# Optimization experiments

Measured on AMD Instinct MI355X. Metric: run time of the kernel, lower is better.

Reference implementation:

```python
import jax, jax.numpy as jnp
import numpy as np

ALPHAS = (0.1, 0.3, 0.5)
WEIGHTS = (0.5, 0.3, 0.2)

B, T, D = 32, 8192, 64


def setup_inputs() -> dict:
    key = jax.random.key(0)
    k1, k2 = jax.random.split(key)
    pred = jax.random.normal(k1, (B, T, D), dtype=jnp.float32)
    target = jax.random.normal(k2, (B, T, D), dtype=jnp.float32)
    return {"pred": pred, "target": target}


def _ema(x, alpha):
    # ema_0 = x_0 ; ema_i = alpha*x_i + (1-alpha)*ema_{i-1}
    # Express each step as affine op (mult, add) and compose with an
    # associative scan along the time axis (dim=1):  y_i = mult*y_{i-1} + add.
    mult = jnp.full(x.shape, 1.0 - alpha, dtype=x.dtype).at[:, 0].set(0.0)
    add = (alpha * x).at[:, 0].set(x[:, 0])

    def combine(c1, c2):  # apply c1 first, then c2
        a1, b1 = c1
        a2, b2 = c2
        return (a1 * a2, b1 * a2 + b2)

    _, ema = jax.lax.associative_scan(combine, (mult, add), axis=1)
    return ema


def _scale_loss(pred, target, alpha):
    pe = _ema(pred, alpha)   # [B, T, D]
    te = _ema(target, alpha)
    pd = pe[:, 1:] - pe[:, :-1]
    td = te[:, 1:] - te[:, :-1]
    mismatch = jnp.sign(pd) != jnp.sign(td)
    step_err = jnp.square(pe[:, 1:] - te[:, 1:])
    masked = jnp.where(mismatch, step_err, jnp.zeros_like(step_err))
    return masked.mean(axis=1)  # [B, D]


def reference(pred, target):
    loss = sum(w * _scale_loss(pred, target, a) for a, w in zip(ALPHAS, WEIGHTS))
    return loss.mean()  # reduction='mean'
```

## Files before the change

kernel.cpp:

```cpp
#include <hip/hip_runtime.h>


namespace {
constexpr int BB  = 32;
constexpr int TT  = 8192;
constexpr int DD  = 64;
constexpr int CH  = 64;
constexpr int WU  = 32;
constexpr int NCH = TT / CH;
constexpr int WPB = 4;
constexpr int BT  = 16;
constexpr float INV_NORM = 1.0f / (8191.0f * 2048.0f);
}

__global__ void zero_out_kernel(float* o) { o[0] = 0.0f; }

__device__ __forceinline__ void load16(const float* __restrict__ p,
                                       const float* __restrict__ q, int bt,
                                       float (&xs)[BT], float (&ys)[BT]) {
#pragma unroll
  for (int i = 0; i < BT; ++i) {
    xs[i] = p[(bt + i) * DD];
    ys[i] = q[(bt + i) * DD];
  }
}

__device__ __forceinline__ void warm16_a0(const float (&xs)[BT], const float (&ys)[BT],
                                          float& pe0, float& te0) {
#pragma unroll
  for (int i = 0; i < BT; ++i) {
    pe0 = fmaf(0.1f, xs[i] - pe0, pe0);
    te0 = fmaf(0.1f, ys[i] - te0, te0);
  }
}

__device__ __forceinline__ void warm16_all(const float (&xs)[BT], const float (&ys)[BT],
    float& pe0, float& te0, float& pe1, float& te1, float& pe2, float& te2) {
#pragma unroll
  for (int i = 0; i < BT; ++i) {
    pe0 = fmaf(0.1f, xs[i] - pe0, pe0);  te0 = fmaf(0.1f, ys[i] - te0, te0);
    pe1 = fmaf(0.3f, xs[i] - pe1, pe1);  te1 = fmaf(0.3f, ys[i] - te1, te1);
    pe2 = fmaf(0.5f, xs[i] - pe2, pe2);  te2 = fmaf(0.5f, ys[i] - te2, te2);
  }
}

__device__ __forceinline__ void step1(float xx, float yy, float a, float w,
                                      float& pe, float& te, float& acc) {
  float dx = xx - pe;
  float dy = yy - te;
  pe = fmaf(a, dx, pe);
  te = fmaf(a, dy, te);
  float e   = pe - te;
  float sel = (dx * dy < 0.0f) ? w : 0.0f;
  acc = fmaf(sel, e * e, acc);
}

__device__ __forceinline__ void acc16_all(const float (&xs)[BT], const float (&ys)[BT],
    float& pe0, float& te0, float& pe1, float& te1, float& pe2, float& te2,
    float& acc) {
#pragma unroll
  for (int i = 0; i < BT; ++i) {
    step1(xs[i], ys[i], 0.1f, 0.5f, pe0, te0, acc);
    step1(xs[i], ys[i], 0.3f, 0.3f, pe1, te1, acc);
    step1(xs[i], ys[i], 0.5f, 0.2f, pe2, te2, acc);
  }
}

__global__ __launch_bounds__(256, 4) void ms_trend_loss_kernel(
    const float* __restrict__ pred, const float* __restrict__ targ,
    float* __restrict__ out) {
  const int lane = threadIdx.x & 63;
  const int wave = threadIdx.x >> 6;
  const int unit = blockIdx.x * WPB + wave;
  const int b = unit >> 7;
  const int c = unit & 127;
  const int s = c * CH;
  const int start = (c == 0) ? 0 : (s - WU);

  const float* p = pred + (b * TT + start) * DD + lane;
  const float* q = targ + (b * TT + start) * DD + lane;

  float pe0, pe1, pe2, te0, te1, te2;
  float acc = 0.0f;
  float xa[BT], ya[BT], xb[BT], yb[BT];

  if (c == 0) {
    load16(p, q, 0, xa, ya);
    load16(p, q, BT, xb, yb);
    pe0 = pe1 = pe2 = xa[0];
    te0 = te1 = te2 = ya[0];
    acc16_all(xa, ya, pe0, te0, pe1, te1, pe2, te2, acc);
    load16(p, q, 2 * BT, xa, ya);
    acc16_all(xb, yb, pe0, te0, pe1, te1, pe2, te2, acc);
    load16(p, q, 3 * BT, xb, yb);
    acc16_all(xa, ya, pe0, te0, pe1, te1, pe2, te2, acc);
    acc16_all(xb, yb, pe0, te0, pe1, te1, pe2, te2, acc);
  } else {
    load16(p, q, 0, xa, ya);
    load16(p, q, BT, xb, yb);
    pe0 = xa[0];
    te0 = ya[0];
    warm16_a0(xa, ya, pe0, te0);
    load16(p, q, 2 * BT, xa, ya);
    pe1 = pe2 = xb[0];
    te1 = te2 = yb[0];
    warm16_all(xb, yb, pe0, te0, pe1, te1, pe2, te2);
    load16(p, q, 3 * BT, xb, yb);
    acc16_all(xa, ya, pe0, te0, pe1, te1, pe2, te2, acc);
    load16(p, q, 4 * BT, xa, ya);
    acc16_all(xb, yb, pe0, te0, pe1, te1, pe2, te2, acc);
    load16(p, q, 5 * BT, xb, yb);
    acc16_all(xa, ya, pe0, te0, pe1, te1, pe2, te2, acc);
    acc16_all(xb, yb, pe0, te0, pe1, te1, pe2, te2, acc);
  }

#pragma unroll
  for (int off = 32; off > 0; off >>= 1) acc += __shfl_down(acc, off);
  __shared__ float sred[WPB];
  if (lane == 0) sred[wave] = acc;
  __syncthreads();
  if (threadIdx.x == 0) {
    float t = sred[0] + sred[1] + sred[2] + sred[3];
    atomicAdd(out, t * INV_NORM);
  }
}

extern "C" void kernel_launch(void* const* d_in, const int* in_sizes, int n_in,
                              void* d_out, int out_size, void* d_ws, size_t ws_size,
                              hipStream_t stream) {
  (void)in_sizes; (void)n_in; (void)out_size; (void)d_ws; (void)ws_size;
  const float* pred = (const float*)d_in[0];
  const float* targ = (const float*)d_in[1];
  float* out = (float*)d_out;

  zero_out_kernel<<<1, 1, 0, stream>>>(out);
  ms_trend_loss_kernel<<<BB * NCH / WPB, 256, 0, stream>>>(pred, targ, out);
}
```

Before: 146.3 us.

## Stream inputs through LDS via async global_load_lds double buffering

Replaces per-lane register loads of 16-row batches with asynchronous global-to-LDS copies (16-byte per lane) into a per-wave double-buffered shared tile of 8 rows. Each wave waits on vmcnt, runs the EMA recurrence reading from LDS, then issues the next batch. The goal is wider, fully coalesced loads with fewer VGPRs and better overlap of memory and compute. The cost is extra LDS traffic, explicit waitcnt handling, and the occupancy hint being dropped from launch bounds.

```diff
diff --git a/kernel.cpp b/kernel.cpp
--- a/kernel.cpp
+++ b/kernel.cpp
@@ -9,38 +9,51 @@
 constexpr int WU  = 32;
 constexpr int NCH = TT / CH;
 constexpr int WPB = 4;
-constexpr int BT  = 16;
+constexpr int BT  = 8;
 constexpr float INV_NORM = 1.0f / (8191.0f * 2048.0f);
 }
 
+typedef const __attribute__((address_space(1))) void* gas_ptr;
+typedef __attribute__((address_space(3))) void* las_ptr;
+
 __global__ void zero_out_kernel(float* o) { o[0] = 0.0f; }
 
-__device__ __forceinline__ void load16(const float* __restrict__ p,
-                                       const float* __restrict__ q, int bt,
-                                       float (&xs)[BT], float (&ys)[BT]) {
+#define WAIT_V4() do { asm volatile("s_waitcnt vmcnt(4)" ::: "memory"); \
+                       __builtin_amdgcn_sched_barrier(0); } while (0)
+#define WAIT_V0() do { asm volatile("s_waitcnt vmcnt(0)" ::: "memory"); \
+                       __builtin_amdgcn_sched_barrier(0); } while (0)
+#define WAIT_LG() do { asm volatile("s_waitcnt lgkmcnt(0)" ::: "memory"); \
+                       __builtin_amdgcn_sched_barrier(0); } while (0)
+
+__device__ __forceinline__ void issue_batch(const float* gx, const float* gy,
+                                            float* lx, float* ly) {
 #pragma unroll
-  for (int i = 0; i < BT; ++i) {
-    xs[i] = p[(bt + i) * DD];
-    ys[i] = q[(bt + i) * DD];
+  for (int r = 0; r < 2; ++r) {
+    __builtin_amdgcn_global_load_lds((gas_ptr)(gx + r * 4 * DD),
+                                     (las_ptr)(lx + r * 4 * DD), 16, 0, 0);
+    __builtin_amdgcn_global_load_lds((gas_ptr)(gy + r * 4 * DD),
+                                     (las_ptr)(ly + r * 4 * DD), 16, 0, 0);
   }
 }
 
-__device__ __forceinline__ void warm16_a0(const float (&xs)[BT], const float (&ys)[BT],
-                                          float& pe0, float& te0) {
+__device__ __forceinline__ void warm8_a0(const float* tx, const float* ty,
+                                         float& pe0, float& te0) {
 #pragma unroll
   for (int i = 0; i < BT; ++i) {
-    pe0 = fmaf(0.1f, xs[i] - pe0, pe0);
-    te0 = fmaf(0.1f, ys[i] - te0, te0);
+    float xx = tx[i * DD], yy = ty[i * DD];
+    pe0 = fmaf(0.1f, xx - pe0, pe0);
+    te0 = fmaf(0.1f, yy - te0, te0);
   }
 }
 
-__device__ __forceinline__ void warm16_all(const float (&xs)[BT], const float (&ys)[BT],
+__device__ __forceinline__ void warm8_all(const float* tx, const float* ty,
     float& pe0, float& te0, float& pe1, float& te1, float& pe2, float& te2) {
 #pragma unroll
   for (int i = 0; i < BT; ++i) {
-    pe0 = fmaf(0.1f, xs[i] - pe0, pe0);  te0 = fmaf(0.1f, ys[i] - te0, te0);
-    pe1 = fmaf(0.3f, xs[i] - pe1, pe1);  te1 = fmaf(0.3f, ys[i] - te1, te1);
-    pe2 = fmaf(0.5f, xs[i] - pe2, pe2);  te2 = fmaf(0.5f, ys[i] - te2, te2);
+    float xx = tx[i * DD], yy = ty[i * DD];
+    pe0 = fmaf(0.1f, xx - pe0, pe0);  te0 = fmaf(0.1f, yy - te0, te0);
+    pe1 = fmaf(0.3f, xx - pe1, pe1);  te1 = fmaf(0.3f, yy - te1, te1);
+    pe2 = fmaf(0.5f, xx - pe2, pe2);  te2 = fmaf(0.5f, yy - te2, te2);
   }
 }
 
@@ -55,20 +68,22 @@
   acc = fmaf(sel, e * e, acc);
 }
 
-__device__ __forceinline__ void acc16_all(const float (&xs)[BT], const float (&ys)[BT],
+__device__ __forceinline__ void acc8(const float* tx, const float* ty,
     float& pe0, float& te0, float& pe1, float& te1, float& pe2, float& te2,
     float& acc) {
 #pragma unroll
   for (int i = 0; i < BT; ++i) {
-    step1(xs[i], ys[i], 0.1f, 0.5f, pe0, te0, acc);
-    step1(xs[i], ys[i], 0.3f, 0.3f, pe1, te1, acc);
-    step1(xs[i], ys[i], 0.5f, 0.2f, pe2, te2, acc);
+    float xx = tx[i * DD], yy = ty[i * DD];
+    step1(xx, yy, 0.1f, 0.5f, pe0, te0, acc);
+    step1(xx, yy, 0.3f, 0.3f, pe1, te1, acc);
+    step1(xx, yy, 0.5f, 0.2f, pe2, te2, acc);
   }
 }
 
-__global__ __launch_bounds__(256, 4) void ms_trend_loss_kernel(
-    const float* __restrict__ pred, const float* __restrict__ targ,
-    float* __restrict__ out) {
+__global__ void __launch_bounds__(256)
+ms_trend_loss_kernel(const float* __restrict__ pred,
+                     const float* __restrict__ targ,
+                     float* __restrict__ out) {
   const int lane = threadIdx.x & 63;
   const int wave = threadIdx.x >> 6;
   const int unit = blockIdx.x * WPB + wave;
@@ -77,41 +92,69 @@
   const int s = c * CH;
   const int start = (c == 0) ? 0 : (s - WU);
 
-  const float* p = pred + (b * TT + start) * DD + lane;
-  const float* q = targ + (b * TT + start) * DD + lane;
+  const float* gx = pred + (b * TT + start) * DD + lane * 4;
+  const float* gy = targ + (b * TT + start) * DD + lane * 4;
+
+  __shared__ float tile[WPB][2][2][BT * DD];
+#define LX(k) (&tile[wave][(k) & 1][0][0])
+#define LY(k) (&tile[wave][(k) & 1][1][0])
+#define TX(k) (&tile[wave][(k) & 1][0][lane])
+#define TY(k) (&tile[wave][(k) & 1][1][lane])
 
   float pe0, pe1, pe2, te0, te1, te2;
   float acc = 0.0f;
-  float xa[BT], ya[BT], xb[BT], yb[BT];
+
+  issue_batch(gx, gy, LX(0), LY(0));
+  issue_batch(gx + BT * DD, gy + BT * DD, LX(1), LY(1));
 
   if (c == 0) {
-    load16(p, q, 0, xa, ya);
-    load16(p, q, BT, xb, yb);
-    pe0 = pe1 = pe2 = xa[0];
-    te0 = te1 = te2 = ya[0];
-    acc16_all(xa, ya, pe0, te0, pe1, te1, pe2, te2, acc);
-    load16(p, q, 2 * BT, xa, ya);
-    acc16_all(xb, yb, pe0, te0, pe1, te1, pe2, te2, acc);
-    load16(p, q, 3 * BT, xb, yb);
-    acc16_all(xa, ya, pe0, te0, pe1, te1, pe2, te2, acc);
-    acc16_all(xb, yb, pe0, te0, pe1, te1, pe2, te2, acc);
+    WAIT_V4();
+    pe0 = pe1 = pe2 = TX(0)[0];
+    te0 = te1 = te2 = TY(0)[0];
+    acc8(TX(0), TY(0), pe0, te0, pe1, te1, pe2, te2, acc);
+    WAIT_LG();
+    issue_batch(gx + 2 * BT * DD, gy + 2 * BT * DD, LX(0), LY(0));
+    for (int k = 1; k < 6; ++k) {
+      WAIT_V4();
+      acc8(TX(k), TY(k), pe0, te0, pe1, te1, pe2, te2, acc);
+      WAIT_LG();
+      issue_batch(gx + (k + 2) * BT * DD, gy + (k + 2) * BT * DD, LX(k), LY(k));
+    }
+    WAIT_V4();
+    acc8(TX(6), TY(6), pe0, te0, pe1, te1, pe2, te2, acc);
+    WAIT_V0();
+    acc8(TX(7), TY(7), pe0, te0, pe1, te1, pe2, te2, acc);
   } else {
-    load16(p, q, 0, xa, ya);
-    load16(p, q, BT, xb, yb);
-    pe0 = xa[0];
-    te0 = ya[0];
-    warm16_a0(xa, ya, pe0, te0);
-    load16(p, q, 2 * BT, xa, ya);
-    pe1 = pe2 = xb[0];
-    te1 = te2 = yb[0];
-    warm16_all(xb, yb, pe0, te0, pe1, te1, pe2, te2);
-    load16(p, q, 3 * BT, xb, yb);
-    acc16_all(xa, ya, pe0, te0, pe1, te1, pe2, te2, acc);
-    load16(p, q, 4 * BT, xa, ya);
-    acc16_all(xb, yb, pe0, te0, pe1, te1, pe2, te2, acc);
-    load16(p, q, 5 * BT, xb, yb);
-    acc16_all(xa, ya, pe0, te0, pe1, te1, pe2, te2, acc);
-    acc16_all(xb, yb, pe0, te0, pe1, te1, pe2, te2, acc);
+    WAIT_V4();
+    pe0 = TX(0)[0];
+    te0 = TY(0)[0];
+    warm8_a0(TX(0), TY(0), pe0, te0);
+    WAIT_LG();
+    issue_batch(gx + 2 * BT * DD, gy + 2 * BT * DD, LX(0), LY(0));
+    WAIT_V4();
+    warm8_a0(TX(1), TY(1), pe0, te0);
+    WAIT_LG();
+    issue_batch(gx + 3 * BT * DD, gy + 3 * BT * DD, LX(1), LY(1));
+    WAIT_V4();
+    pe1 = pe2 = TX(2)[0];
+    te1 = te2 = TY(2)[0];
+    warm8_all(TX(2), TY(2), pe0, te0, pe1, te1, pe2, te2);
+    WAIT_LG();
+    issue_batch(gx + 4 * BT * DD, gy + 4 * BT * DD, LX(2), LY(2));
+    WAIT_V4();
+    warm8_all(TX(3), TY(3), pe0, te0, pe1, te1, pe2, te2);
+    WAIT_LG();
+    issue_batch(gx + 5 * BT * DD, gy + 5 * BT * DD, LX(3), LY(3));
+    for (int k = 4; k < 10; ++k) {
+      WAIT_V4();
+      acc8(TX(k), TY(k), pe0, te0, pe1, te1, pe2, te2, acc);
+      WAIT_LG();
+      issue_batch(gx + (k + 2) * BT * DD, gy + (k + 2) * BT * DD, LX(k), LY(k));
+    }
+    WAIT_V4();
+    acc8(TX(10), TY(10), pe0, te0, pe1, te1, pe2, te2, acc);
+    WAIT_V0();
+    acc8(TX(11), TY(11), pe0, te0, pe1, te1, pe2, te2, acc);
   }
 
 #pragma unroll
```

Result: slower. 157.3 us (+7.5%).
